# Performance work log

Hardware: AMD Instinct MI355X
Metric: run time of the kernel (lower is better)

Reference implementation:

```python
import jax, jax.numpy as jnp
import numpy as np

WINDOW = (2, 6, 12)  # (Wz, Wy, Wx)
HEADS = 6


def _position_index(window):
    Wz, Wy, Wx = window
    cz, cy, cx = np.arange(Wz), np.arange(Wy), np.arange(Wx)
    coords = np.stack(np.meshgrid(cz, cy, cx, indexing='ij'))  # [3, Wz, Wy, Wx]
    cf = coords.reshape(3, -1)                                  # [3, N]
    rel = cf[:, :, None] - cf[:, None, :]                       # [3, N, N]
    rel = rel.transpose(1, 2, 0).astype(np.int64)               # [N, N, 3]
    rel[:, :, 0] += Wz - 1
    rel[:, :, 1] += Wy - 1
    rel[:, :, 2] += Wx - 1
    rel[:, :, 0] *= 2 * Wy - 1
    return jnp.asarray(rel.sum(-1).reshape(-1))                 # [N*N]


def setup_inputs() -> dict:
    key = jax.random.key(0)
    ks = jax.random.split(key, 7)
    dim, N, B_, nW = 192, 144, 1024, 512
    table_rows = (2 * WINDOW[2] - 1) * (2 * WINDOW[1] - 1) * (2 * WINDOW[0] - 1)  # 759
    return {
        'x': jax.random.normal(ks[0], (B_, N, dim), jnp.float32),
        'mask': jax.random.normal(ks[1], (nW, N, N), jnp.float32),
        'w_qkv': jax.random.normal(ks[2], (dim, 3 * dim), jnp.float32) * 0.02,
        'b_qkv': jax.random.normal(ks[3], (3 * dim,), jnp.float32) * 0.02,
        'w_o': jax.random.normal(ks[4], (dim, dim), jnp.float32) * 0.02,
        'b_o': jax.random.normal(ks[5], (dim,), jnp.float32) * 0.02,
        'bias_table': jax.random.normal(ks[6], (table_rows, 1, HEADS), jnp.float32) * 0.02,
    }


def reference(x, mask, w_qkv, b_qkv, w_o, b_o, bias_table):
    B_, N, dim = x.shape
    H = HEADS
    hd = dim // H
    scale = hd ** -0.5

    qkv = x @ w_qkv + b_qkv                              # [B_, N, 3*dim]
    qkv = qkv.reshape(B_, N, 3, H, hd).transpose(2, 0, 3, 1, 4)
    q, k, v = qkv[0], qkv[1], qkv[2]                     # [B_, H, N, hd]

    attn = jnp.einsum('bhnd,bhmd->bhnm', q * scale, k)   # [B_, H, N, N]

    pos_idx = _position_index(WINDOW)                    # [N*N] int constant
    bias = bias_table[pos_idx].reshape(N, N, H).transpose(2, 0, 1)  # [H, N, N]
    attn = attn + bias[None]

    nW = mask.shape[0]
    attn = attn.reshape(B_ // nW, nW, H, N, N) + mask[None, :, None]
    attn = jax.nn.softmax(attn.reshape(B_, H, N, N), axis=-1)

    out = jnp.einsum('bhnm,bhmd->bhnd', attn, v)         # [B_, H, N, hd]
    out = out.transpose(0, 2, 1, 3).reshape(B_, N, dim)
    return out @ w_o + b_o
```

## Files before the change

### kernel.cpp

```cpp
#include <hip/hip_runtime.h>

typedef __attribute__((ext_vector_type(4))) float  f32x4;
typedef __attribute__((ext_vector_type(4))) float  float4v;
typedef __attribute__((ext_vector_type(4))) short  short4v;
typedef __attribute__((ext_vector_type(8))) short  short8v;
typedef __attribute__((ext_vector_type(8))) __bf16 bf16x8;

union Frag { short4v h[2]; short8v s8; };

__device__ __forceinline__ short f2bf(float f) {
  unsigned u = __builtin_bit_cast(unsigned, f);
  u = (u + 0x7fffu + ((u >> 16) & 1u)) >> 16;
  return (short)u;
}

__device__ __forceinline__ f32x4 mfma_bf16(const Frag& a, const Frag& b, f32x4 c) {
  return __builtin_amdgcn_mfma_f32_16x16x32_bf16(
      __builtin_bit_cast(bf16x8, a.s8), __builtin_bit_cast(bf16x8, b.s8), c, 0, 0, 0);
}

__device__ __forceinline__ int poscode(int i) {
  int z = (i >= 72) ? 1 : 0;
  int rem = i - 72 * z;
  int y = rem / 12;
  return 11 * z + y + (rem - 12 * y);
}

__device__ __forceinline__ int kperm(int r) {
  return (r & 16) ? (((r - 16) >> 2) * 8 + 4 + (r & 3)) : ((r >> 2) * 8 + (r & 3));
}

__global__ __launch_bounds__(256) void k_transpose_w(
    const float* __restrict__ w_qkv, const float* __restrict__ w_o,
    short* __restrict__ wtq, short* __restrict__ wto) {
  int idx = blockIdx.x * 256 + threadIdx.x;
  if (idx < 110592) {
    int k = idx / 576, c = idx % 576;
    int kp = (k & ~31) + kperm(k & 31);
    wtq[c * 192 + kp] = f2bf(w_qkv[idx]);
  } else {
    int j = idx - 110592;
    int k = j / 192, c = j % 192;
    wto[c * 192 + k] = f2bf(w_o[j]);
  }
}

__global__ __launch_bounds__(256) void k_bias(
    const float* __restrict__ btab, float* __restrict__ bias6) {
  int idx = blockIdx.x * 256 + threadIdx.x;
  if (idx >= 124416) return;
  int h = idx / 20736, r = idx % 20736, m = r / 144, n = r % 144;
  bias6[idx] = btab[(poscode(m) - poscode(n) + 27) * 6 + h];
}

__global__ __launch_bounds__(256, 2) void k_qkv(
    const float* __restrict__ x, const float* __restrict__ bqkv,
    const short* __restrict__ wtq, short* __restrict__ qkv) {
  __shared__ short a_lds[64][200];
  __shared__ short bT[576][40];
  const int tid = threadIdx.x;
  const int lane = tid & 63, wv = tid >> 6;
  const int l15 = lane & 15, lg = lane >> 4;
  const int row0 = blockIdx.x * 64;

#pragma unroll
  for (int i = 0; i < 12; ++i) {
    int flat = tid + 256 * i;
    int r = flat / 48, c4 = flat % 48;
    float4v xv = *(const float4v*)&x[(size_t)(row0 + r) * 192 + c4 * 4];
    short4v sv = { f2bf(xv[0]), f2bf(xv[1]), f2bf(xv[2]), f2bf(xv[3]) };
    int k = c4 * 4, rr = k & 31;
    int pos = (k & ~31) + ((rr & 16) ? (((rr - 16) >> 2) * 8 + 4) : ((rr >> 2) * 8));
    *(short4v*)&a_lds[r][pos] = sv;
  }

  f32x4 acc[36];
#pragma unroll
  for (int i = 0; i < 36; ++i) acc[i] = f32x4{0.f, 0.f, 0.f, 0.f};

  for (int kc = 0; kc < 6; ++kc) {
    __syncthreads();
#pragma unroll
    for (int i = 0; i < 9; ++i) {
      int flat = tid + 256 * i;
      int c = flat >> 2, j = flat & 3;
      *(short8v*)&bT[c][j * 8] = *(const short8v*)&wtq[c * 192 + kc * 32 + j * 8];
    }
    __syncthreads();
    Frag a;
    a.s8 = *(const short8v*)&a_lds[wv * 16 + l15][kc * 32 + lg * 8];
#pragma unroll
    for (int cf = 0; cf < 36; ++cf) {
      Frag bw;
      bw.s8 = *(const short8v*)&bT[cf * 16 + l15][lg * 8];
      acc[cf] = mfma_bf16(bw, a, acc[cf]);
    }
  }

  const int g = row0 + wv * 16 + l15;
  const int b_ = g / 144, n = g - b_ * 144;
#pragma unroll
  for (int cf = 0; cf < 36; ++cf) {
    int c0 = cf * 16 + lg * 4;
    int part = c0 / 192, rem = c0 % 192;
    int h = rem >> 5, d0 = rem & 31;
    int q4 = d0 >> 2;
    int dd0 = (part == 2) ? d0 : ((q4 < 4) ? q4 * 8 : (q4 - 4) * 8 + 4);
    float4v bias4 = *(const float4v*)&bqkv[c0];
    float scale = (part == 0) ? 0.17677669529663687f : 1.0f;
    short4v sv = { f2bf((acc[cf][0] + bias4[0]) * scale),
                   f2bf((acc[cf][1] + bias4[1]) * scale),
                   f2bf((acc[cf][2] + bias4[2]) * scale),
                   f2bf((acc[cf][3] + bias4[3]) * scale) };
    *(short4v*)&qkv[(size_t)((part * 1024 + b_) * 6 + h) * 4608 + n * 32 + dd0] = sv;
  }
}

__global__ __launch_bounds__(512, 2) void k_attn(
    const short* __restrict__ qkv, const float* __restrict__ mask,
    const float* __restrict__ bias6, float* __restrict__ out) {
  __shared__ short k_l[6][144][40];
  __shared__ short vt[6][32][168];
  const int tid = threadIdx.x;
  const int lane = tid & 63, wv = tid >> 6;
  const int l15 = lane & 15, lg = lane >> 4;

  const int bid = blockIdx.x;
  const int b = ((bid >> 4) << 3) + (bid & 7) + (((bid >> 3) & 1) << 9);
  const int wm = b & 511;

  const size_t kbase = (size_t)(1024 + b) * 6 * 4608;
#pragma unroll
  for (int i = 0; i < 7; ++i) {
    int flat = tid + 512 * i;
    if (flat < 3456) {
      int h = flat / 576, r = flat % 576;
      int n = r >> 2, j8 = (r & 3) * 8;
      *(short8v*)&k_l[h][n][j8] =
          *(const short8v*)&qkv[kbase + (size_t)h * 4608 + n * 32 + j8];
    }
  }
#pragma unroll
  for (int i = 0; i < 6; ++i) {
    int flat = tid + 512 * i;
    int h = flat / 512, r = flat & 511;
    int d = r >> 4, jj = r & 15;
    vt[h][d][128 + (jj >> 2) * 8 + 4 + (jj & 3)] = 0;
  }
  const size_t vbase = (size_t)(2048 + b) * 6 * 4608;
#pragma unroll
  for (int i = 0; i < 14; ++i) {
    int flat = tid + 512 * i;
    if (flat < 6912) {
      int h = flat / 1152, r = flat % 1152;
      int n = r >> 3, d4 = (r & 7) * 4;
      short4v vv = *(const short4v*)&qkv[vbase + (size_t)h * 4608 + n * 32 + d4];
      int np = (n & ~31) + kperm(n & 31);
      vt[h][d4 + 0][np] = vv[0];
      vt[h][d4 + 1][np] = vv[1];
      vt[h][d4 + 2][np] = vv[2];
      vt[h][d4 + 3][np] = vv[3];
    }
  }
  __syncthreads();

  const float* maskw = &mask[(size_t)wm * 20736];
  const size_t qb = (size_t)b * 6 * 4608;

  f32x4 mrow[9];
  int q = 0;
  for (int unit = 0; unit < 7; ++unit) {
    int t, h;
    if (unit < 6) { t = wv; h = unit; }
    else { if (wv >= 6) break; t = 8; h = wv; }
    if (unit == 0 || unit == 6) {
      q = t * 16 + l15;
#pragma unroll
      for (int cf = 0; cf < 9; ++cf)
        mrow[cf] = *(const float4v*)&maskw[q * 144 + cf * 16 + lg * 4];
    }

    Frag aq;
    aq.s8 = *(const short8v*)&qkv[qb + (size_t)h * 4608 + q * 32 + lg * 8];

    f32x4 s[9];
#pragma unroll
    for (int cf = 0; cf < 9; ++cf) {
      Frag bk;
      bk.s8 = *(const short8v*)&k_l[h][cf * 16 + l15][lg * 8];
      s[cf] = mfma_bf16(bk, aq, f32x4{0.f, 0.f, 0.f, 0.f});
    }
    const float* brow = &bias6[(size_t)(h * 144 + q) * 144];
#pragma unroll
    for (int cf = 0; cf < 9; ++cf) {
      float4v bv = *(const float4v*)&brow[cf * 16 + lg * 4];
      s[cf] += mrow[cf] + bv;
    }

    float mx = s[0][0];
#pragma unroll
    for (int cf = 0; cf < 9; ++cf)
#pragma unroll
      for (int reg = 0; reg < 4; ++reg) mx = fmaxf(mx, s[cf][reg]);
    mx = fmaxf(mx, __shfl_xor(mx, 16, 64));
    mx = fmaxf(mx, __shfl_xor(mx, 32, 64));
    float sum = 0.f;
#pragma unroll
    for (int cf = 0; cf < 9; ++cf)
#pragma unroll
      for (int reg = 0; reg < 4; ++reg) {
        float e = __expf(s[cf][reg] - mx);
        s[cf][reg] = e;
        sum += e;
      }
    sum += __shfl_xor(sum, 16, 64);
    sum += __shfl_xor(sum, 32, 64);
    const float rinv = 1.0f / sum;
#pragma unroll
    for (int cf = 0; cf < 9; ++cf)
#pragma unroll
      for (int reg = 0; reg < 4; ++reg) s[cf][reg] *= rinv;

    f32x4 o0 = {0.f, 0.f, 0.f, 0.f}, o1 = {0.f, 0.f, 0.f, 0.f};
#pragma unroll
    for (int kc = 0; kc < 5; ++kc) {
      Frag p, b0, b1;
      p.h[0] = short4v{ f2bf(s[2 * kc][0]), f2bf(s[2 * kc][1]),
                        f2bf(s[2 * kc][2]), f2bf(s[2 * kc][3]) };
      p.h[1] = (kc < 4)
          ? short4v{ f2bf(s[2 * kc + 1][0]), f2bf(s[2 * kc + 1][1]),
                     f2bf(s[2 * kc + 1][2]), f2bf(s[2 * kc + 1][3]) }
          : short4v{0, 0, 0, 0};
      b0.s8 = *(const short8v*)&vt[h][l15][kc * 32 + lg * 8];
      b1.s8 = *(const short8v*)&vt[h][16 + l15][kc * 32 + lg * 8];
      o0 = mfma_bf16(b0, p, o0);
      o1 = mfma_bf16(b1, p, o1);
    }
    const size_t base = (size_t)(b * 144 + q) * 192 + h * 32;
    *(float4v*)&out[base + lg * 4]      = o0;
    *(float4v*)&out[base + 16 + lg * 4] = o1;
  }
}

__global__ __launch_bounds__(256, 2) void k_oproj(
    float* __restrict__ io, const float* __restrict__ bo,
    const short* __restrict__ wto) {
  __shared__ short a_lds[64][200];
  __shared__ short bT[192][40];
  const int tid = threadIdx.x;
  const int lane = tid & 63, wv = tid >> 6;
  const int l15 = lane & 15, lg = lane >> 4;
  const int row0 = blockIdx.x * 64;

#pragma unroll
  for (int i = 0; i < 12; ++i) {
    int flat = tid + 256 * i;
    int r = flat / 48, c4 = flat % 48;
    float4v xv = *(const float4v*)&io[(size_t)(row0 + r) * 192 + c4 * 4];
    short4v sv = { f2bf(xv[0]), f2bf(xv[1]), f2bf(xv[2]), f2bf(xv[3]) };
    *(short4v*)&a_lds[r][c4 * 4] = sv;
  }

  f32x4 acc[12];
#pragma unroll
  for (int i = 0; i < 12; ++i) acc[i] = f32x4{0.f, 0.f, 0.f, 0.f};

  for (int kc = 0; kc < 6; ++kc) {
    __syncthreads();
#pragma unroll
    for (int i = 0; i < 6; ++i) {
      int flat = tid + 256 * i;
      int c = flat >> 3, kk = (flat & 7) << 2;
      *(short4v*)&bT[c][kk] = *(const short4v*)&wto[c * 192 + kc * 32 + kk];
    }
    __syncthreads();
    Frag a;
    a.h[0] = *(const short4v*)&a_lds[wv * 16 + l15][kc * 32 + lg * 4];
    a.h[1] = *(const short4v*)&a_lds[wv * 16 + l15][kc * 32 + lg * 4 + 16];
#pragma unroll
    for (int cf = 0; cf < 12; ++cf) {
      Frag bw;
      bw.h[0] = *(const short4v*)&bT[cf * 16 + l15][lg * 4];
      bw.h[1] = *(const short4v*)&bT[cf * 16 + l15][lg * 4 + 16];
      acc[cf] = mfma_bf16(bw, a, acc[cf]);
    }
  }

  const int g = row0 + wv * 16 + l15;
#pragma unroll
  for (int cf = 0; cf < 12; ++cf) {
    int c0 = cf * 16 + lg * 4;
    float4v bias4 = *(const float4v*)&bo[c0];
    *(float4v*)&io[(size_t)g * 192 + c0] = acc[cf] + bias4;
  }
}

extern "C" void kernel_launch(void* const* d_in, const int* in_sizes, int n_in,
                              void* d_out, int out_size, void* d_ws, size_t ws_size,
                              hipStream_t stream) {
  const float* x    = (const float*)d_in[0];
  const float* mask = (const float*)d_in[1];
  const float* wqkv = (const float*)d_in[2];
  const float* bqkv = (const float*)d_in[3];
  const float* wo   = (const float*)d_in[4];
  const float* bo   = (const float*)d_in[5];
  const float* btab = (const float*)d_in[6];
  float* out = (float*)d_out;

  short* wtq   = (short*)d_ws;
  short* wto   = wtq + 110592;
  short* qkv   = wto + 36864;
  float* bias6 = (float*)(qkv + 84934656);

  k_transpose_w<<<576, 256, 0, stream>>>(wqkv, wo, wtq, wto);
  k_bias<<<486, 256, 0, stream>>>(btab, bias6);
  k_qkv<<<2304, 256, 0, stream>>>(x, bqkv, wtq, qkv);
  k_attn<<<1024, 512, 0, stream>>>(qkv, mask, bias6, out);
  k_oproj<<<2304, 256, 0, stream>>>(out, bo, wto);
}
```

Baseline: 269.7 us.

## Retile QKV GEMM, split attention by head groups, use packed bf16 conversions

The QKV projection now tiles 128 rows by 288 columns per block, using two A fragments per B fragment load, with an XCD-aware block swizzle. Attention blocks now handle three heads instead of six, which doubles the grid and halves LDS so more blocks fit per CU. Softmax normalization is deferred to after the PV matmul, and float-to-bf16 conversion uses the hardware v_cvt_pk_bf16_f32 instruction instead of manual rounding. Each attention block now does a smaller serial unit loop, and the Q/K/V staging and mask rows are fetched by twice as many blocks.

```diff
diff --git a/kernel.cpp b/kernel.cpp
--- a/kernel.cpp
+++ b/kernel.cpp
@@ -4,14 +4,27 @@
 typedef __attribute__((ext_vector_type(4))) float  float4v;
 typedef __attribute__((ext_vector_type(4))) short  short4v;
 typedef __attribute__((ext_vector_type(8))) short  short8v;
+typedef __attribute__((ext_vector_type(2))) unsigned uint2v;
 typedef __attribute__((ext_vector_type(8))) __bf16 bf16x8;
 
-union Frag { short4v h[2]; short8v s8; };
+union Frag { short4v h[2]; short8v s8; unsigned u[4]; };
+union BF4  { uint2v u2; short4v s4; };
 
 __device__ __forceinline__ short f2bf(float f) {
   unsigned u = __builtin_bit_cast(unsigned, f);
   u = (u + 0x7fffu + ((u >> 16) & 1u)) >> 16;
   return (short)u;
+}
+
+__device__ __forceinline__ unsigned cvt_pk_bf16(float a, float b) {
+  unsigned r;
+  asm("v_cvt_pk_bf16_f32 %0, %1, %2" : "=v"(r) : "v"(a), "v"(b));
+  return r;
+}
+__device__ __forceinline__ short4v f4_to_bf4(float4v v) {
+  BF4 r;
+  r.u2 = uint2v{ cvt_pk_bf16(v[0], v[1]), cvt_pk_bf16(v[2], v[3]) };
+  return r.s4;
 }
 
 __device__ __forceinline__ f32x4 mfma_bf16(const Frag& a, const Frag& b, f32x4 c) {
@@ -56,84 +69,97 @@
 __global__ __launch_bounds__(256, 2) void k_qkv(
     const float* __restrict__ x, const float* __restrict__ bqkv,
     const short* __restrict__ wtq, short* __restrict__ qkv) {
-  __shared__ short a_lds[64][200];
-  __shared__ short bT[576][40];
+  __shared__ short a_lds[128][200];
+  __shared__ short bT[288][40];
   const int tid = threadIdx.x;
   const int lane = tid & 63, wv = tid >> 6;
   const int l15 = lane & 15, lg = lane >> 4;
-  const int row0 = blockIdx.x * 64;
-
-#pragma unroll
-  for (int i = 0; i < 12; ++i) {
+
+  const int did = blockIdx.x;
+  const int vid = (did & 7) * 288 + (did >> 3);
+  const int row0 = (vid >> 1) * 128;
+  const int col0 = (vid & 1) * 288;
+
+#pragma unroll
+  for (int i = 0; i < 24; ++i) {
     int flat = tid + 256 * i;
     int r = flat / 48, c4 = flat % 48;
     float4v xv = *(const float4v*)&x[(size_t)(row0 + r) * 192 + c4 * 4];
-    short4v sv = { f2bf(xv[0]), f2bf(xv[1]), f2bf(xv[2]), f2bf(xv[3]) };
     int k = c4 * 4, rr = k & 31;
     int pos = (k & ~31) + ((rr & 16) ? (((rr - 16) >> 2) * 8 + 4) : ((rr >> 2) * 8));
-    *(short4v*)&a_lds[r][pos] = sv;
-  }
-
-  f32x4 acc[36];
-#pragma unroll
-  for (int i = 0; i < 36; ++i) acc[i] = f32x4{0.f, 0.f, 0.f, 0.f};
+    *(short4v*)&a_lds[r][pos] = f4_to_bf4(xv);
+  }
+
+  f32x4 acc[2][18];
+#pragma unroll
+  for (int ai = 0; ai < 2; ++ai)
+#pragma unroll
+    for (int i = 0; i < 18; ++i) acc[ai][i] = f32x4{0.f, 0.f, 0.f, 0.f};
 
   for (int kc = 0; kc < 6; ++kc) {
     __syncthreads();
 #pragma unroll
-    for (int i = 0; i < 9; ++i) {
+    for (int i = 0; i < 5; ++i) {
       int flat = tid + 256 * i;
-      int c = flat >> 2, j = flat & 3;
-      *(short8v*)&bT[c][j * 8] = *(const short8v*)&wtq[c * 192 + kc * 32 + j * 8];
+      if (flat < 1152) {
+        int c = flat >> 2, j = flat & 3;
+        *(short8v*)&bT[c][j * 8] =
+            *(const short8v*)&wtq[(col0 + c) * 192 + kc * 32 + j * 8];
+      }
     }
     __syncthreads();
-    Frag a;
-    a.s8 = *(const short8v*)&a_lds[wv * 16 + l15][kc * 32 + lg * 8];
-#pragma unroll
-    for (int cf = 0; cf < 36; ++cf) {
+    Frag a0, a1;
+    a0.s8 = *(const short8v*)&a_lds[wv * 32 + l15][kc * 32 + lg * 8];
+    a1.s8 = *(const short8v*)&a_lds[wv * 32 + 16 + l15][kc * 32 + lg * 8];
+#pragma unroll
+    for (int cf = 0; cf < 18; ++cf) {
       Frag bw;
       bw.s8 = *(const short8v*)&bT[cf * 16 + l15][lg * 8];
-      acc[cf] = mfma_bf16(bw, a, acc[cf]);
-    }
-  }
-
-  const int g = row0 + wv * 16 + l15;
-  const int b_ = g / 144, n = g - b_ * 144;
-#pragma unroll
-  for (int cf = 0; cf < 36; ++cf) {
-    int c0 = cf * 16 + lg * 4;
-    int part = c0 / 192, rem = c0 % 192;
-    int h = rem >> 5, d0 = rem & 31;
-    int q4 = d0 >> 2;
-    int dd0 = (part == 2) ? d0 : ((q4 < 4) ? q4 * 8 : (q4 - 4) * 8 + 4);
-    float4v bias4 = *(const float4v*)&bqkv[c0];
-    float scale = (part == 0) ? 0.17677669529663687f : 1.0f;
-    short4v sv = { f2bf((acc[cf][0] + bias4[0]) * scale),
-                   f2bf((acc[cf][1] + bias4[1]) * scale),
-                   f2bf((acc[cf][2] + bias4[2]) * scale),
-                   f2bf((acc[cf][3] + bias4[3]) * scale) };
-    *(short4v*)&qkv[(size_t)((part * 1024 + b_) * 6 + h) * 4608 + n * 32 + dd0] = sv;
-  }
-}
-
-__global__ __launch_bounds__(512, 2) void k_attn(
+      acc[0][cf] = mfma_bf16(bw, a0, acc[0][cf]);
+      acc[1][cf] = mfma_bf16(bw, a1, acc[1][cf]);
+    }
+  }
+
+#pragma unroll
+  for (int ai = 0; ai < 2; ++ai) {
+    const int g = row0 + wv * 32 + ai * 16 + l15;
+    const int b_ = g / 144, n = g - b_ * 144;
+#pragma unroll
+    for (int cf = 0; cf < 18; ++cf) {
+      int c0 = col0 + cf * 16 + lg * 4;
+      int part = c0 / 192, rem = c0 % 192;
+      int h = rem >> 5, d0 = rem & 31;
+      int q4 = d0 >> 2;
+      int dd0 = (part == 2) ? d0 : ((q4 < 4) ? q4 * 8 : (q4 - 4) * 8 + 4);
+      float4v bias4 = *(const float4v*)&bqkv[c0];
+      float scale = (part == 0) ? 0.17677669529663687f : 1.0f;
+      float4v t = (acc[ai][cf] + bias4) * scale;
+      *(short4v*)&qkv[(size_t)((part * 1024 + b_) * 6 + h) * 4608 + n * 32 + dd0] =
+          f4_to_bf4(t);
+    }
+  }
+}
+
+__global__ __launch_bounds__(512, 4) void k_attn(
     const short* __restrict__ qkv, const float* __restrict__ mask,
     const float* __restrict__ bias6, float* __restrict__ out) {
-  __shared__ short k_l[6][144][40];
-  __shared__ short vt[6][32][168];
+  __shared__ short k_l[3][144][40];
+  __shared__ short vt[3][32][168];
   const int tid = threadIdx.x;
   const int lane = tid & 63, wv = tid >> 6;
   const int l15 = lane & 15, lg = lane >> 4;
 
-  const int bid = blockIdx.x;
-  const int b = ((bid >> 4) << 3) + (bid & 7) + (((bid >> 3) & 1) << 9);
-  const int wm = b & 511;
-
-  const size_t kbase = (size_t)(1024 + b) * 6 * 4608;
-#pragma unroll
-  for (int i = 0; i < 7; ++i) {
+  const int did = blockIdx.x;
+  const int vid = (did & 7) * 256 + (did >> 3);
+  const int wm = vid >> 2, r4 = vid & 3;
+  const int b = wm + (r4 >> 1) * 512;
+  const int h0 = (r4 & 1) * 3;
+
+  const size_t kbase = (size_t)((1024 + b) * 6 + h0) * 4608;
+#pragma unroll
+  for (int i = 0; i < 4; ++i) {
     int flat = tid + 512 * i;
-    if (flat < 3456) {
+    if (flat < 1728) {
       int h = flat / 576, r = flat % 576;
       int n = r >> 2, j8 = (r & 3) * 8;
       *(short8v*)&k_l[h][n][j8] =
@@ -141,17 +167,17 @@
     }
   }
 #pragma unroll
-  for (int i = 0; i < 6; ++i) {
+  for (int i = 0; i < 3; ++i) {
     int flat = tid + 512 * i;
     int h = flat / 512, r = flat & 511;
     int d = r >> 4, jj = r & 15;
     vt[h][d][128 + (jj >> 2) * 8 + 4 + (jj & 3)] = 0;
   }
-  const size_t vbase = (size_t)(2048 + b) * 6 * 4608;
-#pragma unroll
-  for (int i = 0; i < 14; ++i) {
+  const size_t vbase = (size_t)((2048 + b) * 6 + h0) * 4608;
+#pragma unroll
+  for (int i = 0; i < 7; ++i) {
     int flat = tid + 512 * i;
-    if (flat < 6912) {
+    if (flat < 3456) {
       int h = flat / 1152, r = flat % 1152;
       int n = r >> 3, d4 = (r & 7) * 4;
       short4v vv = *(const short4v*)&qkv[vbase + (size_t)h * 4608 + n * 32 + d4];
@@ -165,15 +191,15 @@
   __syncthreads();
 
   const float* maskw = &mask[(size_t)wm * 20736];
-  const size_t qb = (size_t)b * 6 * 4608;
+  const size_t qb = (size_t)(b * 6 + h0) * 4608;
 
   f32x4 mrow[9];
   int q = 0;
-  for (int unit = 0; unit < 7; ++unit) {
-    int t, h;
-    if (unit < 6) { t = wv; h = unit; }
-    else { if (wv >= 6) break; t = 8; h = wv; }
-    if (unit == 0 || unit == 6) {
+  for (int unit = 0; unit < 4; ++unit) {
+    int t, hl;
+    if (unit < 3) { t = wv; hl = unit; }
+    else { if (wv >= 3) break; t = 8; hl = wv; }
+    if (unit == 0 || unit == 3) {
       q = t * 16 + l15;
 #pragma unroll
       for (int cf = 0; cf < 9; ++cf)
@@ -181,16 +207,16 @@
     }
 
     Frag aq;
-    aq.s8 = *(const short8v*)&qkv[qb + (size_t)h * 4608 + q * 32 + lg * 8];
+    aq.s8 = *(const short8v*)&qkv[qb + (size_t)hl * 4608 + q * 32 + lg * 8];
 
     f32x4 s[9];
 #pragma unroll
     for (int cf = 0; cf < 9; ++cf) {
       Frag bk;
-      bk.s8 = *(const short8v*)&k_l[h][cf * 16 + l15][lg * 8];
+      bk.s8 = *(const short8v*)&k_l[hl][cf * 16 + l15][lg * 8];
       s[cf] = mfma_bf16(bk, aq, f32x4{0.f, 0.f, 0.f, 0.f});
     }
-    const float* brow = &bias6[(size_t)(h * 144 + q) * 144];
+    const float* brow = &bias6[(size_t)((h0 + hl) * 144 + q) * 144];
 #pragma unroll
     for (int cf = 0; cf < 9; ++cf) {
       float4v bv = *(const float4v*)&brow[cf * 16 + lg * 4];
@@ -216,27 +242,27 @@
     sum += __shfl_xor(sum, 16, 64);
     sum += __shfl_xor(sum, 32, 64);
     const float rinv = 1.0f / sum;
-#pragma unroll
-    for (int cf = 0; cf < 9; ++cf)
-#pragma unroll
-      for (int reg = 0; reg < 4; ++reg) s[cf][reg] *= rinv;
 
     f32x4 o0 = {0.f, 0.f, 0.f, 0.f}, o1 = {0.f, 0.f, 0.f, 0.f};
 #pragma unroll
     for (int kc = 0; kc < 5; ++kc) {
       Frag p, b0, b1;
-      p.h[0] = short4v{ f2bf(s[2 * kc][0]), f2bf(s[2 * kc][1]),
-                        f2bf(s[2 * kc][2]), f2bf(s[2 * kc][3]) };
-      p.h[1] = (kc < 4)
-          ? short4v{ f2bf(s[2 * kc + 1][0]), f2bf(s[2 * kc + 1][1]),
-                     f2bf(s[2 * kc + 1][2]), f2bf(s[2 * kc + 1][3]) }
-          : short4v{0, 0, 0, 0};
-      b0.s8 = *(const short8v*)&vt[h][l15][kc * 32 + lg * 8];
-      b1.s8 = *(const short8v*)&vt[h][16 + l15][kc * 32 + lg * 8];
+      p.u[0] = cvt_pk_bf16(s[2 * kc][0], s[2 * kc][1]);
+      p.u[1] = cvt_pk_bf16(s[2 * kc][2], s[2 * kc][3]);
+      if (kc < 4) {
+        p.u[2] = cvt_pk_bf16(s[2 * kc + 1][0], s[2 * kc + 1][1]);
+        p.u[3] = cvt_pk_bf16(s[2 * kc + 1][2], s[2 * kc + 1][3]);
+      } else {
+        p.u[2] = 0; p.u[3] = 0;
+      }
+      b0.s8 = *(const short8v*)&vt[hl][l15][kc * 32 + lg * 8];
+      b1.s8 = *(const short8v*)&vt[hl][16 + l15][kc * 32 + lg * 8];
       o0 = mfma_bf16(b0, p, o0);
       o1 = mfma_bf16(b1, p, o1);
     }
-    const size_t base = (size_t)(b * 144 + q) * 192 + h * 32;
+    o0 *= rinv;
+    o1 *= rinv;
+    const size_t base = (size_t)(b * 144 + q) * 192 + (h0 + hl) * 32;
     *(float4v*)&out[base + lg * 4]      = o0;
     *(float4v*)&out[base + 16 + lg * 4] = o1;
   }
@@ -257,8 +283,7 @@
     int flat = tid + 256 * i;
     int r = flat / 48, c4 = flat % 48;
     float4v xv = *(const float4v*)&io[(size_t)(row0 + r) * 192 + c4 * 4];
-    short4v sv = { f2bf(xv[0]), f2bf(xv[1]), f2bf(xv[2]), f2bf(xv[3]) };
-    *(short4v*)&a_lds[r][c4 * 4] = sv;
+    *(short4v*)&a_lds[r][c4 * 4] = f4_to_bf4(xv);
   }
 
   f32x4 acc[12];
@@ -315,6 +340,6 @@
   k_transpose_w<<<576, 256, 0, stream>>>(wqkv, wo, wtq, wto);
   k_bias<<<486, 256, 0, stream>>>(btab, bias6);
   k_qkv<<<2304, 256, 0, stream>>>(x, bqkv, wtq, qkv);
-  k_attn<<<1024, 512, 0, stream>>>(qkv, mask, bias6, out);
+  k_attn<<<2048, 512, 0, stream>>>(qkv, mask, bias6, out);
   k_oproj<<<2304, 256, 0, stream>>>(out, bo, wto);
 }
```

Result: slower. 312.3 us (+15.8%).
